# Performance work log

Measured on AMD Instinct MI355X. Metric: run time of the kernel, lower is better.

Reference implementation:

```python
import jax, jax.numpy as jnp
import numpy as np

EPS = 1e-5  # BatchNorm eps (inference-mode BN with running stats)


def bn(x, g, b, m, v):
    # x: [B,C,H,W]; per-channel affine BN (inference)
    inv = jax.lax.rsqrt(v + EPS)
    return (x - m[None, :, None, None]) * (g * inv)[None, :, None, None] + b[None, :, None, None]


def conv1x1(x, w):
    # x: [B,Ci,H,W], w: [Co,Ci,1,1]
    return jnp.einsum('bchw,oc->bohw', x, w[:, :, 0, 0])


def conv3x3(x, w, b):
    out = jax.lax.conv_general_dilated(
        x, w, window_strides=(1, 1), padding=((1, 1), (1, 1)),
        dimension_numbers=('NCHW', 'OIHW', 'NCHW'))
    return out + b[None, :, None, None]


def deform_conv3x3(x, offset, w):
    # x: [B,C,H,W]; offset: [B,18,H,W] with channel 2k = dy_k, 2k+1 = dx_k
    # w: [Co,C,3,3]; stride=1, pad=1, dilation=1, deformable_groups=1
    B, C, H, W = x.shape
    K = 9
    kidx = jnp.arange(K)
    kdy = (kidx // 3 - 1).astype(x.dtype)  # base kernel y offsets in {-1,0,1}
    kdx = (kidx % 3 - 1).astype(x.dtype)
    off = offset.reshape(B, K, 2, H, W)
    gh = jnp.arange(H, dtype=x.dtype)
    gw = jnp.arange(W, dtype=x.dtype)
    # sampling locations [B,K,H,W]
    py = gh[None, None, :, None] + kdy[None, :, None, None] + off[:, :, 0]
    px = gw[None, None, None, :] + kdx[None, :, None, None] + off[:, :, 1]

    y0 = jnp.floor(py)
    x0 = jnp.floor(px)
    wy1 = py - y0
    wx1 = px - x0
    y0i = y0.astype(jnp.int32)
    x0i = x0.astype(jnp.int32)

    xflat = x.reshape(B, C, H * W)

    def gather(yi, xi):
        valid = ((yi >= 0) & (yi < H) & (xi >= 0) & (xi < W))
        idx = (jnp.clip(yi, 0, H - 1) * W + jnp.clip(xi, 0, W - 1)).reshape(B, 1, -1)
        g = jnp.take_along_axis(xflat, idx, axis=2).reshape(B, C, K, H, W)
        return g * valid[:, None].astype(x.dtype)

    sampled = (
        gather(y0i, x0i) * ((1 - wy1) * (1 - wx1))[:, None]
        + gather(y0i, x0i + 1) * ((1 - wy1) * wx1)[:, None]
        + gather(y0i + 1, x0i) * (wy1 * (1 - wx1))[:, None]
        + gather(y0i + 1, x0i + 1) * (wy1 * wx1)[:, None]
    )  # [B,C,K,H,W]
    return jnp.einsum('bckhw,ock->bohw', sampled, w.reshape(w.shape[0], C, K))


def setup_inputs() -> dict:
    key = jax.random.key(0)
    ks = jax.random.split(key, 20)
    B, Cin, H, W = 2, 1024, 64, 64
    Cb, Cout = 256, 1024

    def msra(k, shape):
        fan_out = shape[0] * int(np.prod(shape[2:]))
        return jax.random.normal(k, shape, jnp.float32) * np.sqrt(2.0 / fan_out)

    inp = {
        'x': jax.random.normal(ks[0], (B, Cin, H, W), jnp.float32),
        'w1': msra(ks[1], (Cb, Cin, 1, 1)),
        'g1': jnp.ones((Cb,)), 'b1': jnp.zeros((Cb,)),
        'm1': jax.random.normal(ks[2], (Cb,)) * 0.1,
        'v1': jax.random.uniform(ks[3], (Cb,)) + 0.5,
        # offset conv (small weights so offsets stay in a realistic range)
        'w_off': msra(ks[4], (18, Cb, 3, 3)) * 0.05,
        'b_off': jnp.zeros((18,)),
        'w2': msra(ks[5], (Cb, Cb, 3, 3)),
        'g2': jnp.ones((Cb,)), 'b2': jnp.zeros((Cb,)),
        'm2': jax.random.normal(ks[6], (Cb,)) * 0.1,
        'v2': jax.random.uniform(ks[7], (Cb,)) + 0.5,
        'w3': msra(ks[8], (Cout, Cb, 1, 1)),
        'g3': jnp.ones((Cout,)), 'b3': jnp.zeros((Cout,)),
        'm3': jax.random.normal(ks[9], (Cout,)) * 0.1,
        'v3': jax.random.uniform(ks[10], (Cout,)) + 0.5,
    }
    return inp


def reference(x, w1, g1, b1, m1, v1, w_off, b_off, w2, g2, b2, m2, v2,
              w3, g3, b3, m3, v3):
    out = jax.nn.relu(bn(conv1x1(x, w1), g1, b1, m1, v1))
    offset = conv3x3(out, w_off, b_off)          # [B,18,H,W]
    out = bn(deform_conv3x3(out, offset, w2), g2, b2, m2, v2)
    out = jax.nn.relu(out)
    out = bn(conv1x1(out, w3), g3, b3, m3, v3)
    out = out + x                                 # identity shortcut (Cin==Cout, stride=1)
    return jax.nn.relu(out)
```

## Files before the change

### kernel.cpp

```cpp
#include <hip/hip_runtime.h>
#include <hip/hip_bf16.h>

#define EPSV 1e-5f

typedef __attribute__((ext_vector_type(4))) float f32x4;
typedef __attribute__((ext_vector_type(8))) short bf16x8;
typedef unsigned short u16;
typedef unsigned int u32;

#define AS1(p) ((const __attribute__((address_space(1))) void*)(p))
#define AS3(p) ((__attribute__((address_space(3))) void*)(p))

__device__ __forceinline__ float bf2f(u16 u) {
    union { u32 i; float f; } x; x.i = ((u32)u) << 16; return x.f;
}
__device__ __forceinline__ u16 f2bf(float f) {
    __hip_bfloat16 h = __float2bfloat16(f);
    return *reinterpret_cast<u16*>(&h);
}

__global__ __launch_bounds__(256) void prep_cvt(const float* __restrict__ w1,
                                                const float* __restrict__ w3,
                                                u16* __restrict__ wb1,
                                                u16* __restrict__ wb3) {
    int i = blockIdx.x * 256 + threadIdx.x;
    const float* src; u16* dst; int j;
    if (i < 65536) { src = w1; dst = wb1; j = i; }
    else           { src = w3; dst = wb3; j = i - 65536; }
    float4 v = ((const float4*)src)[j];
    ushort4 o;
    o.x = f2bf(v.x); o.y = f2bf(v.y); o.z = f2bf(v.z); o.w = f2bf(v.w);
    ((ushort4*)dst)[j] = o;
}

__global__ __launch_bounds__(256) void prep_reorg(const float* __restrict__ w_off,
                                                  const float* __restrict__ w2,
                                                  u16* __restrict__ wOffP,
                                                  u16* __restrict__ wb2d,
                                                  u16* __restrict__ zbuf) {
    const int bz  = blockIdx.x;
    const int tid = threadIdx.x;
    if (bz == 136) { ((u32*)zbuf)[tid] = 0; return; }
    if (bz < 64) {
#pragma unroll
        for (int k = 0; k < 9; k++) {
            float v = (bz < 18) ? w_off[((size_t)(bz * 256 + tid)) * 9 + k] : 0.f;
            wOffP[(size_t)bz * 2304 + k * 256 + tid] = f2bf(v);
        }
        return;
    }
    const int bz2 = bz - 64;
    const int set = bz2 % 18;
    const int kz  = bz2 / 18;
    const int tap = set >> 1, hk = set & 1;
#pragma unroll
    for (int j = 0; j < 4; j++) {
        bf16x8 ov;
#pragma unroll
        for (int kk = 0; kk < 8; kk++) {
            const int ch = kz * 64 + hk * 32 + j * 8 + kk;
            ov[kk] = (short)f2bf(w2[((size_t)(tid * 256 + ch)) * 9 + tap]);
        }
        *(bf16x8*)(wb2d + ((size_t)(bz2 * 4 + j)) * 2048 + tid * 8) = ov;
    }
}

__global__ __launch_bounds__(256) void cvt_x_T(const float* __restrict__ x,
                                               u16* __restrict__ xbT) {
    __shared__ u16 tile[64][72];
    const int tid = threadIdx.x;
    const int hw0 = blockIdx.x << 6;
    const int c0  = blockIdx.y << 6;
    const int b   = blockIdx.z;
    const int cl  = tid >> 4;
    const int hwl = (tid & 15) << 2;
#pragma unroll
    for (int i = 0; i < 4; i++) {
        const int c = cl + i * 16;
        float4 v = *(const float4*)(x + (((size_t)(b * 1024 + c0 + c)) << 12) + hw0 + hwl);
        tile[hwl + 0][c] = f2bf(v.x);
        tile[hwl + 1][c] = f2bf(v.y);
        tile[hwl + 2][c] = f2bf(v.z);
        tile[hwl + 3][c] = f2bf(v.w);
    }
    __syncthreads();
    const int hw  = tid >> 2;
    const int seg = tid & 3;
    u16* dst = xbT + ((size_t)(b * 4096 + hw0 + hw)) * 1024 + c0 + seg * 16;
    const u16* src = &tile[hw][seg * 16];
#pragma unroll
    for (int q = 0; q < 2; q++)
        *(uint4*)(dst + q * 8) = *(const uint4*)(src + q * 8);
}

#define MFMA8(ASP, BSP)                                                          \
    do {                                                                         \
        bf16x8 a0 = *(const bf16x8*)(ASP);                                       \
        bf16x8 a1 = *(const bf16x8*)((ASP) + 512);                               \
        bf16x8 b0 = *(const bf16x8*)(BSP);                                       \
        bf16x8 b1 = *(const bf16x8*)((BSP) + 512);                               \
        bf16x8 b2 = *(const bf16x8*)((BSP) + 1024);                              \
        bf16x8 b3 = *(const bf16x8*)((BSP) + 1536);                              \
        acc[0][0] = __builtin_amdgcn_mfma_f32_16x16x32_bf16(a0, b0, acc[0][0], 0, 0, 0); \
        acc[0][1] = __builtin_amdgcn_mfma_f32_16x16x32_bf16(a0, b1, acc[0][1], 0, 0, 0); \
        acc[0][2] = __builtin_amdgcn_mfma_f32_16x16x32_bf16(a0, b2, acc[0][2], 0, 0, 0); \
        acc[0][3] = __builtin_amdgcn_mfma_f32_16x16x32_bf16(a0, b3, acc[0][3], 0, 0, 0); \
        acc[1][0] = __builtin_amdgcn_mfma_f32_16x16x32_bf16(a1, b0, acc[1][0], 0, 0, 0); \
        acc[1][1] = __builtin_amdgcn_mfma_f32_16x16x32_bf16(a1, b1, acc[1][1], 0, 0, 0); \
        acc[1][2] = __builtin_amdgcn_mfma_f32_16x16x32_bf16(a1, b2, acc[1][2], 0, 0, 0); \
        acc[1][3] = __builtin_amdgcn_mfma_f32_16x16x32_bf16(a1, b3, acc[1][3], 0, 0, 0); \
    } while (0)

#define WAIT_BAR()                                  \
    do {                                            \
        asm volatile("s_waitcnt vmcnt(3)" ::: "memory"); \
        __builtin_amdgcn_s_barrier();               \
        __builtin_amdgcn_sched_barrier(0);          \
    } while (0)

#define POST_BAR()                                  \
    do {                                            \
        __builtin_amdgcn_s_barrier();               \
        __builtin_amdgcn_sched_barrier(0);          \
    } while (0)

template<int MODE>
__global__ __launch_bounds__(256) void gemm_bn(
    const u16* __restrict__ A, const u16* __restrict__ BT,
    const float* __restrict__ g, const float* __restrict__ bb,
    const float* __restrict__ m, const float* __restrict__ v,
    const float* __restrict__ resid, void* __restrict__ out, int K, int Ksub)
{
    extern __shared__ char sm[];

    const int tid  = threadIdx.x;
    const int lane = tid & 63;
    const int wid  = tid >> 6;
    const int n0 = blockIdx.x << 7;
    const int m0 = blockIdx.y << 6;
    const int kBase = blockIdx.z * Ksub;
    const int wr = wid >> 1, wc = wid & 1;
    const int lr = lane & 15, kg = lane >> 4;

    f32x4 acc[2][4] = {};

    const int arow = tid >> 2, aseg = (tid & 3) << 3;
    const u16* aG  = A  + (size_t)(m0 + arow) * K + kBase + aseg;
    const u16* bG0 = BT + (size_t)(n0 + arow) * K + kBase + aseg;
    const u16* bG1 = BT + (size_t)(n0 + 64 + arow) * K + kBase + aseg;

    char* ldsA0  = sm + wid * 1024;
    char* ldsA1  = sm + 4096  + wid * 1024;
    char* ldsB00 = sm + 8192  + wid * 1024;
    char* ldsB01 = sm + 12288 + wid * 1024;
    char* ldsB10 = sm + 16384 + wid * 1024;
    char* ldsB11 = sm + 20480 + wid * 1024;

    const u16* Asp0 = (const u16*)(sm)         + (wr * 32 + lr) * 32 + kg * 8;
    const u16* Asp1 = (const u16*)(sm + 4096)  + (wr * 32 + lr) * 32 + kg * 8;
    const u16* Bsp0 = (const u16*)(sm + 8192)  + (wc * 64 + lr) * 32 + kg * 8;
    const u16* Bsp1 = (const u16*)(sm + 16384) + (wc * 64 + lr) * 32 + kg * 8;

    float sc[2][4], tc[2][4];
#pragma unroll
    for (int mm = 0; mm < 2; mm++)
#pragma unroll
        for (int r = 0; r < 4; r++) {
            const int o = m0 + wr * 32 + mm * 16 + kg * 4 + r;
            const float s = g[o] * rsqrtf(v[o] + EPSV);
            sc[mm][r] = s;
            tc[mm][r] = bb[o] - m[o] * s;
        }
    asm volatile("s_waitcnt vmcnt(0) lgkmcnt(0)" ::: "memory");
    __builtin_amdgcn_sched_barrier(0);

#define ISSUE_G(LA, LB0, LB1, kt)                                                  \
    do {                                                                           \
        __builtin_amdgcn_global_load_lds(AS1(aG + (kt)),  AS3(LA),  16, 0, 0);     \
        __builtin_amdgcn_global_load_lds(AS1(bG0 + (kt)), AS3(LB0), 16, 0, 0);     \
        __builtin_amdgcn_global_load_lds(AS1(bG1 + (kt)), AS3(LB1), 16, 0, 0);     \
    } while (0)

    const int nT = Ksub >> 5;
    ISSUE_G(ldsA0, ldsB00, ldsB01, 0);
    ISSUE_G(ldsA1, ldsB10, ldsB11, 32);

    for (int t = 0; t < nT; t += 2) {
        WAIT_BAR();
        MFMA8(Asp0, Bsp0);
        POST_BAR();
        { const int kn = (t + 2 < nT ? t + 2 : t) << 5;
          ISSUE_G(ldsA0, ldsB00, ldsB01, kn); }
        WAIT_BAR();
        MFMA8(Asp1, Bsp1);
        POST_BAR();
        { const int kn = (t + 3 < nT ? t + 3 : t + 1) << 5;
          ISSUE_G(ldsA1, ldsB10, ldsB11, kn); }
    }
#undef ISSUE_G

    if (MODE == 1) {
        u32* T32 = (u32*)(sm + 24576);
#pragma unroll
        for (int mm = 0; mm < 2; mm++) {
            const int ol = wr * 32 + mm * 16 + kg * 4;
            const int cw0 = ol >> 1;
#pragma unroll
            for (int j = 0; j < 4; j++) {
                const int nl = wc * 64 + j * 16 + lr;
                const int sw = (nl >> 3) & 3;
                float v0 = acc[mm][j][0] * sc[mm][0] + tc[mm][0];
                float v1 = acc[mm][j][1] * sc[mm][1] + tc[mm][1];
                float v2 = acc[mm][j][2] * sc[mm][2] + tc[mm][2];
                float v3 = acc[mm][j][3] * sc[mm][3] + tc[mm][3];
                v0 = v0 > 0.f ? v0 : 0.f; v1 = v1 > 0.f ? v1 : 0.f;
                v2 = v2 > 0.f ? v2 : 0.f; v3 = v3 > 0.f ? v3 : 0.f;
                uint2 pw;
                pw.x = (u32)f2bf(v0) | ((u32)f2bf(v1) << 16);
                pw.y = (u32)f2bf(v2) | ((u32)f2bf(v3) << 16);
                *(uint2*)&T32[nl * 36 + (cw0 ^ (sw << 2))] = pw;
            }
        }
        __syncthreads();
        const int nl = tid >> 1, half = tid & 1;
        const int sw = (nl >> 3) & 3;
        u16* dst = (u16*)out + (size_t)(n0 + nl) * 256 + m0 + half * 32;
#pragma unroll
        for (int q = 0; q < 4; q++) {
            uint4 val = *(const uint4*)&T32[nl * 36 + ((half * 16 + q * 4) ^ (sw << 2))];
            *(uint4*)(dst + q * 8) = val;
        }
    } else {
        float* T = (float*)(sm + 24576);
#pragma unroll
        for (int mm = 0; mm < 2; mm++) {
            const int ol = wr * 32 + mm * 16 + kg * 4;
#pragma unroll
            for (int j = 0; j < 4; j++) {
                const int nl = wc * 64 + j * 16 + lr;
#pragma unroll
                for (int r = 0; r < 4; r++)
                    T[(ol + r) * 132 + nl] = acc[mm][j][r] * sc[mm][r] + tc[mm][r];
            }
        }
        __syncthreads();
        float* O = (float*)out;
        for (int idx = tid; idx < 2048; idx += 256) {
            const int ol  = idx >> 5;
            const int nl4 = (idx & 31) << 2;
            const int n = n0 + nl4;
            const size_t gidx = ((size_t)(n >> 12) << 22) + ((size_t)(m0 + ol) << 12) + (n & 4095);
            float4 rv = *(const float4*)(resid + gidx);
            float4 ov;
            ov.x = T[ol * 132 + nl4 + 0] + rv.x;
            ov.y = T[ol * 132 + nl4 + 1] + rv.y;
            ov.z = T[ol * 132 + nl4 + 2] + rv.z;
            ov.w = T[ol * 132 + nl4 + 3] + rv.w;
            ov.x = ov.x > 0.f ? ov.x : 0.f;
            ov.y = ov.y > 0.f ? ov.y : 0.f;
            ov.z = ov.z > 0.f ? ov.z : 0.f;
            ov.w = ov.w > 0.f ? ov.w : 0.f;
            *(float4*)(O + gidx) = ov;
        }
    }
}

__global__ __launch_bounds__(256) void gemm_off(
    const u16* __restrict__ A,
    const u16* __restrict__ out1T,
    const u16* __restrict__ zbuf,
    float* __restrict__ offsP)
{
    __shared__ char sm[24576];

    const int tid  = threadIdx.x;
    const int lane = tid & 63;
    const int wid  = tid >> 6;
    const int n0 = blockIdx.x << 7;
    const int kz = blockIdx.y;
    const int wr = wid >> 1, wc = wid & 1;
    const int lr = lane & 15, kg = lane >> 4;

    f32x4 acc[2][4] = {};

    const int arow = tid >> 2, aseg = (tid & 3) << 3;
    const u16* aG = A + (size_t)arow * 2304 + aseg;
    const int nB0 = n0 + arow, nB1 = n0 + 64 + arow;
    const int y0r = (nB0 & 4095) >> 6, x0r = nB0 & 63;
    const int y1r = (nB1 & 4095) >> 6, x1r = nB1 & 63;

    char* ldsA0  = sm + wid * 1024;
    char* ldsA1  = sm + 4096  + wid * 1024;
    char* ldsB00 = sm + 8192  + wid * 1024;
    char* ldsB01 = sm + 12288 + wid * 1024;
    char* ldsB10 = sm + 16384 + wid * 1024;
    char* ldsB11 = sm + 20480 + wid * 1024;

    const u16* Asp0 = (const u16*)(sm)         + (wr * 32 + lr) * 32 + kg * 8;
    const u16* Asp1 = (const u16*)(sm + 4096)  + (wr * 32 + lr) * 32 + kg * 8;
    const u16* Bsp0 = (const u16*)(sm + 8192)  + (wc * 64 + lr) * 32 + kg * 8;
    const u16* Bsp1 = (const u16*)(sm + 16384) + (wc * 64 + lr) * 32 + kg * 8;

#define ISSUE_O(LA, LB0, LB1, kt)                                                  \
    do {                                                                           \
        const int tap = (kt) >> 8, c0 = (kt) & 255;                                \
        const int dy = tap / 3 - 1, dx = tap % 3 - 1;                              \
        const int sh = dy * 64 + dx;                                               \
        const bool vv0 = ((unsigned)(y0r + dy) < 64u) && ((unsigned)(x0r + dx) < 64u); \
        const bool vv1 = ((unsigned)(y1r + dy) < 64u) && ((unsigned)(x1r + dx) < 64u); \
        const u16* s0 = vv0 ? out1T + (size_t)(nB0 + sh) * 256 + c0 + aseg : zbuf + aseg; \
        const u16* s1 = vv1 ? out1T + (size_t)(nB1 + sh) * 256 + c0 + aseg : zbuf + aseg; \
        __builtin_amdgcn_global_load_lds(AS1(aG + (kt)), AS3(LA),  16, 0, 0);      \
        __builtin_amdgcn_global_load_lds(AS1(s0),        AS3(LB0), 16, 0, 0);      \
        __builtin_amdgcn_global_load_lds(AS1(s1),        AS3(LB1), 16, 0, 0);      \
    } while (0)

    const int kBase = kz * 384;
    ISSUE_O(ldsA0, ldsB00, ldsB01, kBase);
    ISSUE_O(ldsA1, ldsB10, ldsB11, kBase + 32);

    for (int t = 0; t < 12; t += 2) {
        WAIT_BAR();
        MFMA8(Asp0, Bsp0);
        POST_BAR();
        { const int kn = kBase + ((t + 2 < 12 ? t + 2 : t) << 5);
          ISSUE_O(ldsA0, ldsB00, ldsB01, kn); }
        WAIT_BAR();
        MFMA8(Asp1, Bsp1);
        POST_BAR();
        { const int kn = kBase + ((t + 3 < 12 ? t + 3 : t + 1) << 5);
          ISSUE_O(ldsA1, ldsB10, ldsB11, kn); }
    }
#undef ISSUE_O

    asm volatile("s_waitcnt vmcnt(0)" ::: "memory");

#pragma unroll
    for (int mm = 0; mm < 2; mm++)
#pragma unroll
        for (int r = 0; r < 4; r++) {
            const int o = wr * 32 + mm * 16 + kg * 4 + r;
            if (o < 18) {
#pragma unroll
                for (int j = 0; j < 4; j++) {
                    const int n = n0 + wc * 64 + j * 16 + lr;
                    offsP[(size_t)kz * 147456 +
                          (((size_t)((n >> 12) * 18 + o)) << 12) + (n & 4095)] =
                        acc[mm][j][r];
                }
            }
        }
}

__global__ __launch_bounds__(256) void reduce_offs(
    const float* __restrict__ offsP,
    const float* __restrict__ b_off,
    float* __restrict__ offs)
{
    const int i = blockIdx.x * 256 + threadIdx.x;
    const int ch = (i >> 10) % 18;
    const float bo = b_off[ch];
    float4 s = make_float4(bo, bo, bo, bo);
#pragma unroll
    for (int kz = 0; kz < 6; kz++) {
        float4 v = ((const float4*)(offsP + (size_t)kz * 147456))[i];
        s.x += v.x; s.y += v.y; s.z += v.z; s.w += v.w;
    }
    ((float4*)offs)[i] = s;
}

__global__ __launch_bounds__(256) void gemm_def(
    const u16* __restrict__ wb2d,
    const u16* __restrict__ out1T,
    const float* __restrict__ offs,
    float* __restrict__ P)
{
    extern __shared__ char sm[];
    char*   ldsA0 = sm;
    char*   ldsA1 = sm + 16384;
    char*   ldsB0 = sm + 32768;
    char*   ldsB1 = sm + 36928;
    int4*   s_ofs = (int4*)(sm + 41088);
    float4* s_w   = (float4*)(sm + 50304);

    const int tid  = threadIdx.x;
    const int lane = tid & 63;
    const int wid  = tid >> 6;
    const int n0 = blockIdx.x << 6;
    const int kz = blockIdx.y;
    const int b  = n0 >> 12;
    const int h  = (n0 >> 6) & 63;
    const int lr = lane & 15, kg = lane >> 4;

    for (int p = tid; p < 576; p += 256) {
        const int nl_ = p / 9;
        const int t   = p - nl_ * 9;
        const float dy = offs[(((size_t)(b * 18 + 2 * t)) << 12) + (h << 6) + nl_];
        const float dx = offs[(((size_t)(b * 18 + 2 * t + 1)) << 12) + (h << 6) + nl_];
        const float py = (float)h + (float)(t / 3 - 1) + dy;
        const float px = (float)nl_ + (float)(t % 3 - 1) + dx;
        const float y0f = floorf(py), x0f = floorf(px);
        const int y0 = (int)y0f, x0 = (int)x0f;
        const float wy1 = py - y0f, wx1 = px - x0f;
        const float wy0 = 1.f - wy1, wx0 = 1.f - wx1;
        const int y1 = y0 + 1, x1 = x0 + 1;
        const bool vy0 = (y0 >= 0) && (y0 < 64);
        const bool vy1 = (y1 >= 0) && (y1 < 64);
        const bool vx0 = (x0 >= 0) && (x0 < 64);
        const bool vx1 = (x1 >= 0) && (x1 < 64);
        const int cy0 = min(max(y0, 0), 63), cy1 = min(max(y1, 0), 63);
        const int cx0 = min(max(x0, 0), 63), cx1 = min(max(x1, 0), 63);
        const int rb = b << 12;
        int4 o4; float4 w4;
        o4.x = (rb + (cy0 << 6) + cx0) << 9;  w4.x = wy0 * wx0 * ((vy0 && vx0) ? 1.f : 0.f);
        o4.y = (rb + (cy0 << 6) + cx1) << 9;  w4.y = wy0 * wx1 * ((vy0 && vx1) ? 1.f : 0.f);
        o4.z = (rb + (cy1 << 6) + cx0) << 9;  w4.z = wy1 * wx0 * ((vy1 && vx0) ? 1.f : 0.f);
        o4.w = (rb + (cy1 << 6) + cx1) << 9;  w4.w = wy1 * wx1 * ((vy1 && vx1) ? 1.f : 0.f);
        s_ofs[p] = o4; s_w[p] = w4;
    }
    __syncthreads();

    const int nl = tid >> 2;
    const int q  = tid & 3;
    const u16* aBase = wb2d + (size_t)(kz * 18) * 8192 + tid * 8;
    const char* o1B = (const char*)out1T;
    const int cbQ = kz * 128 + q * 16;

    f32x4 acc[4][4] = {};
    bf16x8 ar0[4], ar1[4], cr0[4], cr1[4];

#define PWC(p_) ((p_) < 18 ? (p_) : 17)

#define LOADR(RI, pt_)                                                             \
    do {                                                                           \
        const u16* ag_ = aBase + (size_t)(pt_) * 8192;                             \
        ar##RI[0] = *(const bf16x8*)(ag_);                                         \
        ar##RI[1] = *(const bf16x8*)(ag_ + 2048);                                  \
        ar##RI[2] = *(const bf16x8*)(ag_ + 4096);                                  \
        ar##RI[3] = *(const bf16x8*)(ag_ + 6144);                                  \
        const int tap_ = (pt_) >> 1, hk_ = (pt_) & 1;                              \
        const int4 o4_ = s_ofs[nl * 9 + tap_];                                     \
        const int cb_ = cbQ + hk_ * 64;                                            \
        cr##RI[0] = *(const bf16x8*)(o1B + o4_.x + cb_);                           \
        cr##RI[1] = *(const bf16x8*)(o1B + o4_.y + cb_);                           \
        cr##RI[2] = *(const bf16x8*)(o1B + o4_.z + cb_);                           \
        cr##RI[3] = *(const bf16x8*)(o1B + o4_.w + cb_);                           \
    } while (0)

#define WRITE_SET(RI, LA, LB, pw_)                                                 \
    do {                                                                           \
        *(bf16x8*)((LA) + 0 * 4096 + tid * 16) = ar##RI[0];                        \
        *(bf16x8*)((LA) + 1 * 4096 + tid * 16) = ar##RI[1];                        \
        *(bf16x8*)((LA) + 2 * 4096 + tid * 16) = ar##RI[2];                        \
        *(bf16x8*)((LA) + 3 * 4096 + tid * 16) = ar##RI[3];                        \
        const float4 w4_ = s_w[nl * 9 + ((pw_) >> 1)];                             \
        bf16x8 pk_;                                                                \
        _Pragma("unroll")                                                          \
        for (int i_ = 0; i_ < 8; i_++) {                                           \
            const float f_ = w4_.x * bf2f((u16)cr##RI[0][i_])                      \
                           + w4_.y * bf2f((u16)cr##RI[1][i_])                      \
                           + w4_.z * bf2f((u16)cr##RI[2][i_])                      \
                           + w4_.w * bf2f((u16)cr##RI[3][i_]);                     \
            pk_[i_] = (short)f2bf(f_);                                             \
        }                                                                          \
        *(bf16x8*)((LB) + q * 1040 + nl * 16) = pk_;                               \
    } while (0)

#define MFMA16(LA, LB)                                                             \
    do {                                                                           \
        bf16x8 av0 = *(const bf16x8*)((LA) + kg * 4096 + (wid * 64 +  0 + lr) * 16); \
        bf16x8 av1 = *(const bf16x8*)((LA) + kg * 4096 + (wid * 64 + 16 + lr) * 16); \
        bf16x8 av2 = *(const bf16x8*)((LA) + kg * 4096 + (wid * 64 + 32 + lr) * 16); \
        bf16x8 av3 = *(const bf16x8*)((LA) + kg * 4096 + (wid * 64 + 48 + lr) * 16); \
        bf16x8 bv0 = *(const bf16x8*)((LB) + kg * 1040 + ( 0 + lr) * 16);          \
        bf16x8 bv1 = *(const bf16x8*)((LB) + kg * 1040 + (16 + lr) * 16);          \
        bf16x8 bv2 = *(const bf16x8*)((LB) + kg * 1040 + (32 + lr) * 16);          \
        bf16x8 bv3 = *(const bf16x8*)((LB) + kg * 1040 + (48 + lr) * 16);          \
        acc[0][0] = __builtin_amdgcn_mfma_f32_16x16x32_bf16(av0, bv0, acc[0][0], 0, 0, 0); \
        acc[0][1] = __builtin_amdgcn_mfma_f32_16x16x32_bf16(av0, bv1, acc[0][1], 0, 0, 0); \
        acc[0][2] = __builtin_amdgcn_mfma_f32_16x16x32_bf16(av0, bv2, acc[0][2], 0, 0, 0); \
        acc[0][3] = __builtin_amdgcn_mfma_f32_16x16x32_bf16(av0, bv3, acc[0][3], 0, 0, 0); \
        acc[1][0] = __builtin_amdgcn_mfma_f32_16x16x32_bf16(av1, bv0, acc[1][0], 0, 0, 0); \
        acc[1][1] = __builtin_amdgcn_mfma_f32_16x16x32_bf16(av1, bv1, acc[1][1], 0, 0, 0); \
        acc[1][2] = __builtin_amdgcn_mfma_f32_16x16x32_bf16(av1, bv2, acc[1][2], 0, 0, 0); \
        acc[1][3] = __builtin_amdgcn_mfma_f32_16x16x32_bf16(av1, bv3, acc[1][3], 0, 0, 0); \
        acc[2][0] = __builtin_amdgcn_mfma_f32_16x16x32_bf16(av2, bv0, acc[2][0], 0, 0, 0); \
        acc[2][1] = __builtin_amdgcn_mfma_f32_16x16x32_bf16(av2, bv1, acc[2][1], 0, 0, 0); \
        acc[2][2] = __builtin_amdgcn_mfma_f32_16x16x32_bf16(av2, bv2, acc[2][2], 0, 0, 0); \
        acc[2][3] = __builtin_amdgcn_mfma_f32_16x16x32_bf16(av2, bv3, acc[2][3], 0, 0, 0); \
        acc[3][0] = __builtin_amdgcn_mfma_f32_16x16x32_bf16(av3, bv0, acc[3][0], 0, 0, 0); \
        acc[3][1] = __builtin_amdgcn_mfma_f32_16x16x32_bf16(av3, bv1, acc[3][1], 0, 0, 0); \
        acc[3][2] = __builtin_amdgcn_mfma_f32_16x16x32_bf16(av3, bv2, acc[3][2], 0, 0, 0); \
        acc[3][3] = __builtin_amdgcn_mfma_f32_16x16x32_bf16(av3, bv3, acc[3][3], 0, 0, 0); \
    } while (0)

#define END_BAR()                                   \
    do {                                            \
        asm volatile("s_waitcnt lgkmcnt(0)" ::: "memory"); \
        __builtin_amdgcn_s_barrier();               \
        __builtin_amdgcn_sched_barrier(0);          \
    } while (0)

    LOADR(0, 0);
    LOADR(1, 1);
    WRITE_SET(0, ldsA0, ldsB0, 0);
    LOADR(0, 2);
    END_BAR();

    for (int t = 0; t < 18; t += 2) {
        WRITE_SET(1, ldsA1, ldsB1, PWC(t + 1));
        LOADR(1, PWC(t + 3));
        MFMA16(ldsA0, ldsB0);
        END_BAR();
        WRITE_SET(0, ldsA0, ldsB0, PWC(t + 2));
        LOADR(0, PWC(t + 4));
        MFMA16(ldsA1, ldsB1);
        END_BAR();
    }
#undef END_BAR
#undef MFMA16
#undef WRITE_SET
#undef LOADR
#undef PWC

    float* Pk = P + (size_t)kz * 2097152;
#pragma unroll
    for (int mf = 0; mf < 4; mf++)
#pragma unroll
        for (int r = 0; r < 4; r++) {
            const int o = wid * 64 + mf * 16 + kg * 4 + r;
#pragma unroll
            for (int nf = 0; nf < 4; nf++) {
                const int n = n0 + nf * 16 + lr;
                Pk[((size_t)o << 13) + n] = acc[mf][nf][r];
            }
        }
}

__global__ __launch_bounds__(256) void reduce_bn(
    const float* __restrict__ P,
    const float* __restrict__ g, const float* __restrict__ bb,
    const float* __restrict__ m, const float* __restrict__ v,
    u16* __restrict__ o2T)
{
    __shared__ u16 tile[64][72];
    const int tid = threadIdx.x;
    const int n0 = blockIdx.x << 6;
    const int m0 = blockIdx.y << 6;

    const int ml = tid >> 2;
    const int ns = (tid & 3) << 4;
    const int o = m0 + ml;
    const float s = g[o] * rsqrtf(v[o] + EPSV);
    const float tcv = bb[o] - m[o] * s;
    const size_t base = ((size_t)o << 13) + n0 + ns;
#pragma unroll
    for (int qq = 0; qq < 4; qq++) {
        float4 a = *(const float4*)(P + base + qq * 4);
        float4 b = *(const float4*)(P + 2097152 + base + qq * 4);
        float4 c = *(const float4*)(P + 2 * 2097152 + base + qq * 4);
        float4 d = *(const float4*)(P + 3 * 2097152 + base + qq * 4);
        float f0 = (a.x + b.x + c.x + d.x) * s + tcv;
        float f1 = (a.y + b.y + c.y + d.y) * s + tcv;
        float f2 = (a.z + b.z + c.z + d.z) * s + tcv;
        float f3 = (a.w + b.w + c.w + d.w) * s + tcv;
        f0 = f0 > 0.f ? f0 : 0.f; f1 = f1 > 0.f ? f1 : 0.f;
        f2 = f2 > 0.f ? f2 : 0.f; f3 = f3 > 0.f ? f3 : 0.f;
        tile[ns + qq * 4 + 0][ml] = f2bf(f0);
        tile[ns + qq * 4 + 1][ml] = f2bf(f1);
        tile[ns + qq * 4 + 2][ml] = f2bf(f2);
        tile[ns + qq * 4 + 3][ml] = f2bf(f3);
    }
    __syncthreads();
    const int nl = tid >> 2, seg = tid & 3;
    u16* dst = o2T + (size_t)(n0 + nl) * 256 + m0 + seg * 16;
    const u16* src = &tile[nl][seg * 16];
#pragma unroll
    for (int qq = 0; qq < 2; qq++)
        *(uint4*)(dst + qq * 8) = *(const uint4*)(src + qq * 8);
}

extern "C" void kernel_launch(void* const* d_in, const int* in_sizes, int n_in,
                              void* d_out, int out_size, void* d_ws, size_t ws_size,
                              hipStream_t stream) {
    const float* x     = (const float*)d_in[0];
    const float* w1    = (const float*)d_in[1];
    const float* g1    = (const float*)d_in[2];
    const float* b1    = (const float*)d_in[3];
    const float* m1    = (const float*)d_in[4];
    const float* v1    = (const float*)d_in[5];
    const float* w_off = (const float*)d_in[6];
    const float* b_off = (const float*)d_in[7];
    const float* w2    = (const float*)d_in[8];
    const float* g2    = (const float*)d_in[9];
    const float* b2    = (const float*)d_in[10];
    const float* m2    = (const float*)d_in[11];
    const float* v2    = (const float*)d_in[12];
    const float* w3    = (const float*)d_in[13];
    const float* g3    = (const float*)d_in[14];
    const float* b3    = (const float*)d_in[15];
    const float* m3    = (const float*)d_in[16];
    const float* v3    = (const float*)d_in[17];
    float* out = (float*)d_out;

    char* ws = (char*)d_ws;
    u16*  xbT   = (u16*)ws;   ws += (size_t)8192 * 1024 * 2;
    u16*  wb1   = (u16*)ws;   ws += (size_t)256 * 1024 * 2;
    u16*  wb3   = (u16*)ws;   ws += (size_t)1024 * 256 * 2;
    u16*  wOffP = (u16*)ws;   ws += (size_t)64 * 2304 * 2;
    u16*  wb2d  = (u16*)ws;   ws += (size_t)72 * 8192 * 2;
    u16*  zbuf  = (u16*)ws;   ws += (size_t)512 * 2;
    u16*  out1T = (u16*)ws;   ws += (size_t)8192 * 256 * 2;
    float* offsP = (float*)ws; ws += (size_t)6 * 147456 * 4;
    float* offs  = (float*)ws; ws += (size_t)147456 * 4;
    u16*  o2T   = (u16*)ws;   ws += (size_t)8192 * 256 * 2;
    float* P    = (float*)ws;  ws += (size_t)4 * 2097152 * 4;

    prep_cvt<<<dim3(512), 256, 0, stream>>>(w1, w3, wb1, wb3);
    prep_reorg<<<dim3(137), 256, 0, stream>>>(w_off, w2, wOffP, wb2d, zbuf);
    cvt_x_T<<<dim3(64, 16, 2), 256, 0, stream>>>(x, xbT);

    gemm_bn<1><<<dim3(64, 4), 256, 24576 + 18432, stream>>>(
        wb1, xbT, g1, b1, m1, v1, nullptr, out1T, 1024, 1024);

    gemm_off<<<dim3(64, 6), 256, 0, stream>>>(wOffP, out1T, zbuf, offsP);

    reduce_offs<<<dim3(144), 256, 0, stream>>>(offsP, b_off, offs);

    gemm_def<<<dim3(128, 4), 256, 59520, stream>>>(wb2d, out1T, offs, P);

    reduce_bn<<<dim3(128, 4), 256, 0, stream>>>(P, g2, b2, m2, v2, o2T);

    gemm_bn<2><<<dim3(64, 16), 256, 24576 + 64 * 132 * 4, stream>>>(
        wb3, o2T, g3, b3, m3, v3, x, out, 256, 256);
}
```

Before: 103.8 us.

## Fuse offset reduction into deform GEMM and load weights directly to registers

Removes the reduce_offs kernel: gemm_def now sums the six split-K partial offset buffers plus bias itself when computing the bilinear sampling tables. The A-operand (deform weights) is loaded straight from global memory into MFMA registers in the fragment layout instead of being staged through LDS, which drops the A buffers and cuts LDS use from about 58KB to 26KB, allowing higher occupancy. The trade-offs are redundant offset summation across the kz blocks and per-wave global loads of A with no LDS sharing.

```diff
diff --git a/kernel.cpp b/kernel.cpp
--- a/kernel.cpp
+++ b/kernel.cpp
@@ -352,36 +352,18 @@
         }
 }
 
-__global__ __launch_bounds__(256) void reduce_offs(
-    const float* __restrict__ offsP,
-    const float* __restrict__ b_off,
-    float* __restrict__ offs)
-{
-    const int i = blockIdx.x * 256 + threadIdx.x;
-    const int ch = (i >> 10) % 18;
-    const float bo = b_off[ch];
-    float4 s = make_float4(bo, bo, bo, bo);
-#pragma unroll
-    for (int kz = 0; kz < 6; kz++) {
-        float4 v = ((const float4*)(offsP + (size_t)kz * 147456))[i];
-        s.x += v.x; s.y += v.y; s.z += v.z; s.w += v.w;
-    }
-    ((float4*)offs)[i] = s;
-}
-
 __global__ __launch_bounds__(256) void gemm_def(
     const u16* __restrict__ wb2d,
     const u16* __restrict__ out1T,
-    const float* __restrict__ offs,
+    const float* __restrict__ offsP,
+    const float* __restrict__ b_off,
     float* __restrict__ P)
 {
     extern __shared__ char sm[];
-    char*   ldsA0 = sm;
-    char*   ldsA1 = sm + 16384;
-    char*   ldsB0 = sm + 32768;
-    char*   ldsB1 = sm + 36928;
-    int4*   s_ofs = (int4*)(sm + 41088);
-    float4* s_w   = (float4*)(sm + 50304);
+    char*   ldsB0 = sm;
+    char*   ldsB1 = sm + 4160;
+    int4*   s_ofs = (int4*)(sm + 8320);
+    float4* s_w   = (float4*)(sm + 17536);
 
     const int tid  = threadIdx.x;
     const int lane = tid & 63;
@@ -393,10 +375,15 @@
     const int lr = lane & 15, kg = lane >> 4;
 
     for (int p = tid; p < 576; p += 256) {
-        const int nl_ = p / 9;
-        const int t   = p - nl_ * 9;
-        const float dy = offs[(((size_t)(b * 18 + 2 * t)) << 12) + (h << 6) + nl_];
-        const float dx = offs[(((size_t)(b * 18 + 2 * t + 1)) << 12) + (h << 6) + nl_];
+        const int t   = p >> 6;
+        const int nl_ = p & 63;
+        const size_t iy = (((size_t)(b * 18 + 2 * t)) << 12) + (h << 6) + nl_;
+        float dy = b_off[2 * t], dx = b_off[2 * t + 1];
+#pragma unroll
+        for (int kzz = 0; kzz < 6; kzz++) {
+            dy += offsP[(size_t)kzz * 147456 + iy];
+            dx += offsP[(size_t)kzz * 147456 + iy + 4096];
+        }
         const float py = (float)h + (float)(t / 3 - 1) + dy;
         const float px = (float)nl_ + (float)(t % 3 - 1) + dx;
         const float y0f = floorf(py), x0f = floorf(px);
@@ -416,28 +403,33 @@
         o4.y = (rb + (cy0 << 6) + cx1) << 9;  w4.y = wy0 * wx1 * ((vy0 && vx1) ? 1.f : 0.f);
         o4.z = (rb + (cy1 << 6) + cx0) << 9;  w4.z = wy1 * wx0 * ((vy1 && vx0) ? 1.f : 0.f);
         o4.w = (rb + (cy1 << 6) + cx1) << 9;  w4.w = wy1 * wx1 * ((vy1 && vx1) ? 1.f : 0.f);
-        s_ofs[p] = o4; s_w[p] = w4;
+        s_ofs[nl_ * 9 + t] = o4; s_w[nl_ * 9 + t] = w4;
     }
     __syncthreads();
 
     const int nl = tid >> 2;
     const int q  = tid & 3;
-    const u16* aBase = wb2d + (size_t)(kz * 18) * 8192 + tid * 8;
+    const u16* aSet  = wb2d + (size_t)(kz * 18) * 8192 + kg * 2048
+                            + (wid * 64 + lr) * 8;
     const char* o1B = (const char*)out1T;
     const int cbQ = kz * 128 + q * 16;
 
     f32x4 acc[4][4] = {};
-    bf16x8 ar0[4], ar1[4], cr0[4], cr1[4];
+    bf16x8 av0[4], av1[4], cr0[4], cr1[4];
 
 #define PWC(p_) ((p_) < 18 ? (p_) : 17)
 
-#define LOADR(RI, pt_)                                                             \
+#define LOADA(RI, pt_)                                                             \
     do {                                                                           \
-        const u16* ag_ = aBase + (size_t)(pt_) * 8192;                             \
-        ar##RI[0] = *(const bf16x8*)(ag_);                                         \
-        ar##RI[1] = *(const bf16x8*)(ag_ + 2048);                                  \
-        ar##RI[2] = *(const bf16x8*)(ag_ + 4096);                                  \
-        ar##RI[3] = *(const bf16x8*)(ag_ + 6144);                                  \
+        const u16* ag_ = aSet + (size_t)(pt_) * 8192;                              \
+        av##RI[0] = *(const bf16x8*)(ag_);                                         \
+        av##RI[1] = *(const bf16x8*)(ag_ + 128);                                   \
+        av##RI[2] = *(const bf16x8*)(ag_ + 256);                                   \
+        av##RI[3] = *(const bf16x8*)(ag_ + 384);                                   \
+    } while (0)
+
+#define LOADC(RI, pt_)                                                             \
+    do {                                                                           \
         const int tap_ = (pt_) >> 1, hk_ = (pt_) & 1;                              \
         const int4 o4_ = s_ofs[nl * 9 + tap_];                                     \
         const int cb_ = cbQ + hk_ * 64;                                            \
@@ -447,12 +439,8 @@
         cr##RI[3] = *(const bf16x8*)(o1B + o4_.w + cb_);                           \
     } while (0)
 
-#define WRITE_SET(RI, LA, LB, pw_)                                                 \
+#define PACKB(RI, LB, pw_)                                                         \
     do {                                                                           \
-        *(bf16x8*)((LA) + 0 * 4096 + tid * 16) = ar##RI[0];                        \
-        *(bf16x8*)((LA) + 1 * 4096 + tid * 16) = ar##RI[1];                        \
-        *(bf16x8*)((LA) + 2 * 4096 + tid * 16) = ar##RI[2];                        \
-        *(bf16x8*)((LA) + 3 * 4096 + tid * 16) = ar##RI[3];                        \
         const float4 w4_ = s_w[nl * 9 + ((pw_) >> 1)];                             \
         bf16x8 pk_;                                                                \
         _Pragma("unroll")                                                          \
@@ -466,32 +454,28 @@
         *(bf16x8*)((LB) + q * 1040 + nl * 16) = pk_;                               \
     } while (0)
 
-#define MFMA16(LA, LB)                                                             \
+#define MFMA16(AV, LB)                                                             \
     do {                                                                           \
-        bf16x8 av0 = *(const bf16x8*)((LA) + kg * 4096 + (wid * 64 +  0 + lr) * 16); \
-        bf16x8 av1 = *(const bf16x8*)((LA) + kg * 4096 + (wid * 64 + 16 + lr) * 16); \
-        bf16x8 av2 = *(const bf16x8*)((LA) + kg * 4096 + (wid * 64 + 32 + lr) * 16); \
-        bf16x8 av3 = *(const bf16x8*)((LA) + kg * 4096 + (wid * 64 + 48 + lr) * 16); \
         bf16x8 bv0 = *(const bf16x8*)((LB) + kg * 1040 + ( 0 + lr) * 16);          \
         bf16x8 bv1 = *(const bf16x8*)((LB) + kg * 1040 + (16 + lr) * 16);          \
         bf16x8 bv2 = *(const bf16x8*)((LB) + kg * 1040 + (32 + lr) * 16);          \
         bf16x8 bv3 = *(const bf16x8*)((LB) + kg * 1040 + (48 + lr) * 16);          \
-        acc[0][0] = __builtin_amdgcn_mfma_f32_16x16x32_bf16(av0, bv0, acc[0][0], 0, 0, 0); \
-        acc[0][1] = __builtin_amdgcn_mfma_f32_16x16x32_bf16(av0, bv1, acc[0][1], 0, 0, 0); \
-        acc[0][2] = __builtin_amdgcn_mfma_f32_16x16x32_bf16(av0, bv2, acc[0][2], 0, 0, 0); \
-        acc[0][3] = __builtin_amdgcn_mfma_f32_16x16x32_bf16(av0, bv3, acc[0][3], 0, 0, 0); \
-        acc[1][0] = __builtin_amdgcn_mfma_f32_16x16x32_bf16(av1, bv0, acc[1][0], 0, 0, 0); \
-        acc[1][1] = __builtin_amdgcn_mfma_f32_16x16x32_bf16(av1, bv1, acc[1][1], 0, 0, 0); \
-        acc[1][2] = __builtin_amdgcn_mfma_f32_16x16x32_bf16(av1, bv2, acc[1][2], 0, 0, 0); \
-        acc[1][3] = __builtin_amdgcn_mfma_f32_16x16x32_bf16(av1, bv3, acc[1][3], 0, 0, 0); \
-        acc[2][0] = __builtin_amdgcn_mfma_f32_16x16x32_bf16(av2, bv0, acc[2][0], 0, 0, 0); \
-        acc[2][1] = __builtin_amdgcn_mfma_f32_16x16x32_bf16(av2, bv1, acc[2][1], 0, 0, 0); \
-        acc[2][2] = __builtin_amdgcn_mfma_f32_16x16x32_bf16(av2, bv2, acc[2][2], 0, 0, 0); \
-        acc[2][3] = __builtin_amdgcn_mfma_f32_16x16x32_bf16(av2, bv3, acc[2][3], 0, 0, 0); \
-        acc[3][0] = __builtin_amdgcn_mfma_f32_16x16x32_bf16(av3, bv0, acc[3][0], 0, 0, 0); \
-        acc[3][1] = __builtin_amdgcn_mfma_f32_16x16x32_bf16(av3, bv1, acc[3][1], 0, 0, 0); \
-        acc[3][2] = __builtin_amdgcn_mfma_f32_16x16x32_bf16(av3, bv2, acc[3][2], 0, 0, 0); \
-        acc[3][3] = __builtin_amdgcn_mfma_f32_16x16x32_bf16(av3, bv3, acc[3][3], 0, 0, 0); \
+        acc[0][0] = __builtin_amdgcn_mfma_f32_16x16x32_bf16(AV[0], bv0, acc[0][0], 0, 0, 0); \
+        acc[0][1] = __builtin_amdgcn_mfma_f32_16x16x32_bf16(AV[0], bv1, acc[0][1], 0, 0, 0); \
+        acc[0][2] = __builtin_amdgcn_mfma_f32_16x16x32_bf16(AV[0], bv2, acc[0][2], 0, 0, 0); \
+        acc[0][3] = __builtin_amdgcn_mfma_f32_16x16x32_bf16(AV[0], bv3, acc[0][3], 0, 0, 0); \
+        acc[1][0] = __builtin_amdgcn_mfma_f32_16x16x32_bf16(AV[1], bv0, acc[1][0], 0, 0, 0); \
+        acc[1][1] = __builtin_amdgcn_mfma_f32_16x16x32_bf16(AV[1], bv1, acc[1][1], 0, 0, 0); \
+        acc[1][2] = __builtin_amdgcn_mfma_f32_16x16x32_bf16(AV[1], bv2, acc[1][2], 0, 0, 0); \
+        acc[1][3] = __builtin_amdgcn_mfma_f32_16x16x32_bf16(AV[1], bv3, acc[1][3], 0, 0, 0); \
+        acc[2][0] = __builtin_amdgcn_mfma_f32_16x16x32_bf16(AV[2], bv0, acc[2][0], 0, 0, 0); \
+        acc[2][1] = __builtin_amdgcn_mfma_f32_16x16x32_bf16(AV[2], bv1, acc[2][1], 0, 0, 0); \
+        acc[2][2] = __builtin_amdgcn_mfma_f32_16x16x32_bf16(AV[2], bv2, acc[2][2], 0, 0, 0); \
+        acc[2][3] = __builtin_amdgcn_mfma_f32_16x16x32_bf16(AV[2], bv3, acc[2][3], 0, 0, 0); \
+        acc[3][0] = __builtin_amdgcn_mfma_f32_16x16x32_bf16(AV[3], bv0, acc[3][0], 0, 0, 0); \
+        acc[3][1] = __builtin_amdgcn_mfma_f32_16x16x32_bf16(AV[3], bv1, acc[3][1], 0, 0, 0); \
+        acc[3][2] = __builtin_amdgcn_mfma_f32_16x16x32_bf16(AV[3], bv2, acc[3][2], 0, 0, 0); \
+        acc[3][3] = __builtin_amdgcn_mfma_f32_16x16x32_bf16(AV[3], bv3, acc[3][3], 0, 0, 0); \
     } while (0)
 
 #define END_BAR()                                   \
@@ -501,26 +485,29 @@
         __builtin_amdgcn_sched_barrier(0);          \
     } while (0)
 
-    LOADR(0, 0);
-    LOADR(1, 1);
-    WRITE_SET(0, ldsA0, ldsB0, 0);
-    LOADR(0, 2);
+    LOADC(0, 0); LOADA(0, 0);
+    LOADC(1, 1); LOADA(1, 1);
+    PACKB(0, ldsB0, 0);
+    LOADC(0, 2);
     END_BAR();
 
     for (int t = 0; t < 18; t += 2) {
-        WRITE_SET(1, ldsA1, ldsB1, PWC(t + 1));
-        LOADR(1, PWC(t + 3));
-        MFMA16(ldsA0, ldsB0);
+        PACKB(1, ldsB1, PWC(t + 1));
+        LOADC(1, PWC(t + 3));
+        MFMA16(av0, ldsB0);
+        LOADA(0, PWC(t + 2));
         END_BAR();
-        WRITE_SET(0, ldsA0, ldsB0, PWC(t + 2));
-        LOADR(0, PWC(t + 4));
-        MFMA16(ldsA1, ldsB1);
+        PACKB(0, ldsB0, PWC(t + 2));
+        LOADC(0, PWC(t + 4));
+        MFMA16(av1, ldsB1);
+        LOADA(1, PWC(t + 3));
         END_BAR();
     }
 #undef END_BAR
 #undef MFMA16
-#undef WRITE_SET
-#undef LOADR
+#undef PACKB
+#undef LOADC
+#undef LOADA
 #undef PWC
 
     float* Pk = P + (size_t)kz * 2097152;
@@ -612,7 +599,6 @@
     u16*  zbuf  = (u16*)ws;   ws += (size_t)512 * 2;
     u16*  out1T = (u16*)ws;   ws += (size_t)8192 * 256 * 2;
     float* offsP = (float*)ws; ws += (size_t)6 * 147456 * 4;
-    float* offs  = (float*)ws; ws += (size_t)147456 * 4;
     u16*  o2T   = (u16*)ws;   ws += (size_t)8192 * 256 * 2;
     float* P    = (float*)ws;  ws += (size_t)4 * 2097152 * 4;
 
@@ -625,9 +611,7 @@
 
     gemm_off<<<dim3(64, 6), 256, 0, stream>>>(wOffP, out1T, zbuf, offsP);
 
-    reduce_offs<<<dim3(144), 256, 0, stream>>>(offsP, b_off, offs);
-
-    gemm_def<<<dim3(128, 4), 256, 59520, stream>>>(wb2d, out1T, offs, P);
+    gemm_def<<<dim3(128, 4), 256, 26752, stream>>>(wb2d, out1T, offsP, b_off, P);
 
     reduce_bn<<<dim3(128, 4), 256, 0, stream>>>(P, g2, b2, m2, v2, o2T);
 
```

Result: no change. 101.9 us (-1.8%).
